# Kernel optimization log

Hardware: AMD Instinct MI355X
Metric: run time of the kernel (lower is better)

Reference implementation:

```python
import jax, jax.numpy as jnp
import numpy as np

NUM_HEADS = 8
NUM_POINTS = 4


def setup_inputs() -> dict:
    key = jax.random.key(0)
    ks = jax.random.split(key, 8)
    B, N, C, H, W = 8, 8192, 256, 128, 128
    HP2 = NUM_HEADS * NUM_POINTS * 2
    HP = NUM_HEADS * NUM_POINTS
    query = jax.random.normal(ks[0], (B, N, C), jnp.float32)
    reference_points = jax.random.uniform(ks[1], (B, N, 2), dtype=jnp.float32)
    value = jax.random.normal(ks[2], (B, C, H, W), jnp.float32)
    # learned params (offset gen is zero-init in the original; use small random
    W_off = jax.random.normal(ks[3], (C, HP2), jnp.float32) * 0.02
    b_off = jnp.zeros((HP2,), jnp.float32)
    W_attn = jax.random.normal(ks[4], (C, HP), jnp.float32) * (1.0 / np.sqrt(C))
    b_attn = jnp.zeros((HP,), jnp.float32)
    W_out = jax.random.normal(ks[5], (C, C), jnp.float32) * (1.0 / np.sqrt(C))
    b_out = jnp.zeros((C,), jnp.float32)
    return dict(query=query, reference_points=reference_points, value=value,
                W_off=W_off, b_off=b_off, W_attn=W_attn, b_attn=b_attn,
                W_out=W_out, b_out=b_out, H=H, W=W)


def reference(query, reference_points, value, W_off, b_off, W_attn, b_attn,
              W_out, b_out, H, W):
    B, N, C = query.shape
    Hh, P = NUM_HEADS, NUM_POINTS
    D = C // Hh

    offset = (query @ W_off + b_off).reshape(B, N, Hh, P, 2)
    attn = jax.nn.softmax((query @ W_attn + b_attn).reshape(B, N, Hh, P), axis=-1)

    # sampling locations in grid_sample convention: (x, y) in [-1, 1]
    ref = reference_points * 2.0 - 1.0
    loc = ref[:, :, None, None, :] + offset  # (B, N, Hh, P, 2)

    # value -> (B, Hh, H*W, D)
    val = value.reshape(B, Hh, D, H, W).transpose(0, 1, 3, 4, 2).reshape(B, Hh, H * W, D)

    # align_corners=False pixel coordinates
    x = (loc[..., 0] + 1.0) * (W * 0.5) - 0.5  # (B, N, Hh, P)
    y = (loc[..., 1] + 1.0) * (H * 0.5) - 0.5
    x0f = jnp.floor(x); y0f = jnp.floor(y)
    wx1 = x - x0f; wy1 = y - y0f
    x0 = x0f.astype(jnp.int32); y0 = y0f.astype(jnp.int32)
    x1 = x0 + 1; y1 = y0 + 1

    def gather(ix, iy, w):
        # bilinear corner gather with zero padding (mask out-of-bounds)
        valid = (ix >= 0) & (ix < W) & (iy >= 0) & (iy < H)
        idx = jnp.clip(iy, 0, H - 1) * W + jnp.clip(ix, 0, W - 1)  # (B,N,Hh,P)
        idx_t = idx.transpose(0, 2, 1, 3).reshape(B, Hh, N * P)
        g = jnp.take_along_axis(val, idx_t[..., None], axis=2)  # (B,Hh,N*P,D)
        g = g.reshape(B, Hh, N, P, D).transpose(0, 2, 1, 3, 4)  # (B,N,Hh,P,D)
        return g * (w * valid)[..., None]

    sampled = (gather(x0, y0, (1 - wx1) * (1 - wy1))
               + gather(x1, y0, wx1 * (1 - wy1))
               + gather(x0, y1, (1 - wx1) * wy1)
               + gather(x1, y1, wx1 * wy1))  # (B,N,Hh,P,D)

    out = jnp.einsum('bnhk,bnhkd->bnhd', attn, sampled).reshape(B, N, C)
    return out @ W_out + b_out
```

## Files before the change

### kernel.cpp

```cpp
#include <hip/hip_runtime.h>
#include <hip/hip_bf16.h>
#include <cstddef>

#define B_  8
#define N_  8192
#define C_  256
#define H_  128
#define W_  128
#define HH  8
#define PP  4
#define DD  32
#define HW  (H_ * W_)

typedef short bf16x8 __attribute__((ext_vector_type(8)));
typedef float f32x4  __attribute__((ext_vector_type(4)));

__global__ __launch_bounds__(256) void kT(const float* __restrict__ value,
                                          __hip_bfloat16* __restrict__ val) {
    __shared__ float tile[32][65];
    const int bh   = blockIdx.y;
    const int pix0 = blockIdx.x * 64;
    const int t    = threadIdx.x;

    const float* src = value + (size_t)bh * 32 * HW + pix0;
#pragma unroll
    for (int i = 0; i < 8; ++i) {
        int d = i * 4 + (t >> 6);
        int p = t & 63;
        tile[d][p] = src[(size_t)d * HW + p];
    }
    __syncthreads();
    __hip_bfloat162* dst =
        (__hip_bfloat162*)(val + ((size_t)bh * HW + pix0) * 32);
#pragma unroll
    for (int j = 0; j < 4; ++j) {
        int p  = j * 16 + (t >> 4);
        int dd = (t & 15) * 2;
        __hip_bfloat162 pk;
        pk.x = __float2bfloat16(tile[dd][p]);
        pk.y = __float2bfloat16(tile[dd + 1][p]);
        dst[p * 16 + (t & 15)] = pk;
    }
}

#define A1_BM 128
#define A1_BK 32

__global__ __launch_bounds__(256) void kA1(const float* __restrict__ query,
                                           const float* __restrict__ refp,
                                           const float* __restrict__ W_off,
                                           const float* __restrict__ b_off,
                                           const float* __restrict__ W_attn,
                                           const float* __restrict__ b_attn,
                                           float4* __restrict__ locattn) {
    __shared__ float At[A1_BK][A1_BM + 4];
    __shared__ float Bo[A1_BK][64];
    __shared__ float Ba[A1_BK][32];

    const int t    = threadIdx.x;
    const int row0 = blockIdx.x * A1_BM;
    const int rg   = t >> 3;
    const int h    = t & 7;

    float accO[4][8];
    float accA[4][4];
#pragma unroll
    for (int r = 0; r < 4; ++r) {
#pragma unroll
        for (int j = 0; j < 8; ++j) accO[r][j] = 0.f;
#pragma unroll
        for (int j = 0; j < 4; ++j) accA[r][j] = 0.f;
    }

    for (int k0 = 0; k0 < C_; k0 += A1_BK) {
        {
            int kq = (t & 7) * 4;
            int ra = t >> 3;
#pragma unroll
            for (int rr = 0; rr < 4; ++rr) {
                int r = ra + rr * 32;
                float4 q = *(const float4*)&query[(size_t)(row0 + r) * C_ + k0 + kq];
                At[kq + 0][r] = q.x;
                At[kq + 1][r] = q.y;
                At[kq + 2][r] = q.z;
                At[kq + 3][r] = q.w;
            }
        }
        {
            int c4 = (t & 15) * 4;
            int kb = t >> 4;
#pragma unroll
            for (int i = 0; i < 2; ++i) {
                int k = kb + i * 16;
                *(float4*)&Bo[k][c4] = *(const float4*)&W_off[(size_t)(k0 + k) * 64 + c4];
            }
        }
        {
            int c4 = (t & 7) * 4;
            int kb = t >> 3;
            *(float4*)&Ba[kb][c4] = *(const float4*)&W_attn[(size_t)(k0 + kb) * 32 + c4];
        }
        __syncthreads();

#pragma unroll
        for (int k = 0; k < A1_BK; ++k) {
            float4 a   = *(const float4*)&At[k][rg * 4];
            float4 bo0 = *(const float4*)&Bo[k][h * 8];
            float4 bo1 = *(const float4*)&Bo[k][h * 8 + 4];
            float4 ba  = *(const float4*)&Ba[k][h * 4];
            float av[4] = {a.x, a.y, a.z, a.w};
            float bO[8] = {bo0.x, bo0.y, bo0.z, bo0.w, bo1.x, bo1.y, bo1.z, bo1.w};
            float bA[4] = {ba.x, ba.y, ba.z, ba.w};
#pragma unroll
            for (int r = 0; r < 4; ++r) {
#pragma unroll
                for (int j = 0; j < 8; ++j) accO[r][j] += av[r] * bO[j];
#pragma unroll
                for (int j = 0; j < 4; ++j) accA[r][j] += av[r] * bA[j];
            }
        }
        __syncthreads();
    }

    float boff[8];
#pragma unroll
    for (int j = 0; j < 8; ++j) boff[j] = b_off[h * 8 + j];
    float batn[4];
#pragma unroll
    for (int j = 0; j < 4; ++j) batn[j] = b_attn[h * 4 + j];

#pragma unroll
    for (int r = 0; r < 4; ++r) {
        int row  = row0 + rg * 4 + r;
        int bb   = row >> 13;
        int nn   = row & 8191;
        float rx = refp[(size_t)row * 2 + 0];
        float ry = refp[(size_t)row * 2 + 1];
        float lg[4];
#pragma unroll
        for (int p = 0; p < 4; ++p) lg[p] = accA[r][p] + batn[p];
        float m = fmaxf(fmaxf(lg[0], lg[1]), fmaxf(lg[2], lg[3]));
        float e[4];
        float s = 0.f;
#pragma unroll
        for (int p = 0; p < 4; ++p) { e[p] = __expf(lg[p] - m); s += e[p]; }
        float inv = 1.f / s;
#pragma unroll
        for (int p = 0; p < 4; ++p) {
            float ox = accO[r][p * 2 + 0] + boff[p * 2 + 0];
            float oy = accO[r][p * 2 + 1] + boff[p * 2 + 1];
            float x  = (rx * 2.f + ox) * (W_ * 0.5f) - 0.5f;
            float y  = (ry * 2.f + oy) * (H_ * 0.5f) - 0.5f;
            locattn[(((size_t)bb * HH + h) * N_ + nn) * PP + p] =
                make_float4(x, y, e[p] * inv, 0.f);
        }
    }
}

__global__ __launch_bounds__(256) void kA2(const float4* __restrict__ locattn,
                                           const __hip_bfloat16* __restrict__ val,
                                           __hip_bfloat16* __restrict__ mid) {
    __shared__ float2 ow[64][4][4];

    const int t  = threadIdx.x;
    const int bh = blockIdx.y;
    const int b  = bh >> 3;
    const int h  = bh & 7;
    const int n0 = blockIdx.x * 64;

    {
        const int r = t >> 2;
        const int p = t & 3;
        float4 L = locattn[((size_t)bh * N_ + n0 + r) * PP + p];
        float x = L.x, y = L.y, a = L.z;
        float xf = floorf(x), yf = floorf(y);
        int x0 = (int)xf, y0 = (int)yf;
        int x1 = x0 + 1, y1 = y0 + 1;
        float wx1 = x - xf, wy1 = y - yf;
        float wx0 = 1.f - wx1, wy0 = 1.f - wy1;
        int cx0 = min(max(x0, 0), W_ - 1);
        int cx1 = min(max(x1, 0), W_ - 1);
        int cy0 = min(max(y0, 0), H_ - 1);
        int cy1 = min(max(y1, 0), H_ - 1);
        bool bx0 = (x0 >= 0) & (x0 < W_);
        bool bx1 = (x1 >= 0) & (x1 < W_);
        bool by0 = (y0 >= 0) & (y0 < H_);
        bool by1 = (y1 >= 0) & (y1 < H_);
        float w00 = a * wx0 * wy0 * ((bx0 & by0) ? 1.f : 0.f);
        float w10 = a * wx1 * wy0 * ((bx1 & by0) ? 1.f : 0.f);
        float w01 = a * wx0 * wy1 * ((bx0 & by1) ? 1.f : 0.f);
        float w11 = a * wx1 * wy1 * ((bx1 & by1) ? 1.f : 0.f);
        ow[r][p][0] = make_float2(__int_as_float(cy0 * W_ + cx0), w00);
        ow[r][p][1] = make_float2(__int_as_float(cy0 * W_ + cx1), w10);
        ow[r][p][2] = make_float2(__int_as_float(cy1 * W_ + cx0), w01);
        ow[r][p][3] = make_float2(__int_as_float(cy1 * W_ + cx1), w11);
    }
    __syncthreads();

    const int d  = t & 31;
    const int rg = t >> 5;
    const __hip_bfloat16* vb = val + (size_t)bh * HW * DD + d;
    __hip_bfloat16* mo = mid + ((size_t)b * N_ + n0) * C_ + h * DD + d;

#pragma unroll
    for (int j = 0; j < 8; ++j) {
        int r = rg * 8 + j;
        const float4* owp = (const float4*)&ow[r][0][0];
        float acc = 0.f;
#pragma unroll
        for (int p = 0; p < 4; ++p) {
            float4 u0 = owp[p * 2 + 0];
            float4 u1 = owp[p * 2 + 1];
            int o00 = __float_as_int(u0.x) * DD;
            int o10 = __float_as_int(u0.z) * DD;
            int o01 = __float_as_int(u1.x) * DD;
            int o11 = __float_as_int(u1.z) * DD;
            acc += u0.y * __bfloat162float(vb[o00]);
            acc += u0.w * __bfloat162float(vb[o10]);
            acc += u1.y * __bfloat162float(vb[o01]);
            acc += u1.w * __bfloat162float(vb[o11]);
        }
        mo[r * C_] = __float2bfloat16(acc);
    }
}

__global__ __launch_bounds__(256) void kW(const float* __restrict__ Wsrc,
                                          __hip_bfloat16* __restrict__ Wt) {
    __shared__ float tile[64][65];
    const int n0 = blockIdx.x * 64;
    const int k0 = blockIdx.y * 64;
    const int t  = threadIdx.x;
#pragma unroll
    for (int i = 0; i < 16; ++i) {
        int kk = i * 4 + (t >> 6);
        int nn = t & 63;
        tile[kk][nn] = Wsrc[(size_t)(k0 + kk) * 256 + n0 + nn];
    }
    __syncthreads();
#pragma unroll
    for (int i = 0; i < 16; ++i) {
        int nn = i * 4 + (t >> 6);
        int kk = t & 63;
        Wt[(size_t)(n0 + nn) * 256 + k0 + kk] = __float2bfloat16(tile[kk][nn]);
    }
}

__global__ __launch_bounds__(256) void kC(const short* __restrict__ mid,
                                          const short* __restrict__ Wt,
                                          const float* __restrict__ bias,
                                          float* __restrict__ out) {
    __shared__ __align__(16) short As[128 * 64];
    __shared__ __align__(16) short Bs[128 * 64];

    const int t    = threadIdx.x;
    const int lane = t & 63;
    const int w    = t >> 6;
    const int wm   = (w & 1) * 64;
    const int wn   = (w >> 1) * 64;
    const int row0 = blockIdx.x * 128;
    const int col0 = blockIdx.y * 128;

    f32x4 acc[4][4];
#pragma unroll
    for (int mt = 0; mt < 4; ++mt)
#pragma unroll
        for (int nt = 0; nt < 4; ++nt)
            acc[mt][nt] = (f32x4){0.f, 0.f, 0.f, 0.f};

    const int sr = t >> 3;
    const int kb = t & 7;

    for (int k0 = 0; k0 < 4; ++k0) {
#pragma unroll
        for (int i = 0; i < 4; ++i) {
            int row  = sr + i * 32;
            int kbs  = (kb ^ (row & 7)) * 8;
            *(uint4*)&As[row * 64 + kbs] =
                *(const uint4*)&mid[(size_t)(row0 + row) * 256 + k0 * 64 + kb * 8];
            *(uint4*)&Bs[row * 64 + kbs] =
                *(const uint4*)&Wt[(size_t)(col0 + row) * 256 + k0 * 64 + kb * 8];
        }
        __syncthreads();

#pragma unroll
        for (int ks = 0; ks < 2; ++ks) {
            const int kq = ks * 4 + (lane >> 4);
            bf16x8 af[4], bf[4];
#pragma unroll
            for (int mt = 0; mt < 4; ++mt) {
                int m = wm + mt * 16 + (lane & 15);
                af[mt] = *(const bf16x8*)&As[m * 64 + (kq ^ (m & 7)) * 8];
            }
#pragma unroll
            for (int nt = 0; nt < 4; ++nt) {
                int n = wn + nt * 16 + (lane & 15);
                bf[nt] = *(const bf16x8*)&Bs[n * 64 + (kq ^ (n & 7)) * 8];
            }
#pragma unroll
            for (int mt = 0; mt < 4; ++mt)
#pragma unroll
                for (int nt = 0; nt < 4; ++nt)
                    acc[mt][nt] = __builtin_amdgcn_mfma_f32_16x16x32_bf16(
                        af[mt], bf[nt], acc[mt][nt], 0, 0, 0);
        }
        __syncthreads();
    }

    const int cq = lane >> 4;
#pragma unroll
    for (int nt = 0; nt < 4; ++nt) {
        int col  = col0 + wn + nt * 16 + (lane & 15);
        float bv = bias[col];
#pragma unroll
        for (int mt = 0; mt < 4; ++mt) {
#pragma unroll
            for (int rI = 0; rI < 4; ++rI) {
                int rowg = row0 + wm + mt * 16 + cq * 4 + rI;
                out[(size_t)rowg * 256 + col] = acc[mt][nt][rI] + bv;
            }
        }
    }
}

extern "C" void kernel_launch(void* const* d_in, const int* in_sizes, int n_in,
                              void* d_out, int out_size, void* d_ws, size_t ws_size,
                              hipStream_t stream) {
    const float* query  = (const float*)d_in[0];
    const float* refp   = (const float*)d_in[1];
    const float* value  = (const float*)d_in[2];
    const float* W_off  = (const float*)d_in[3];
    const float* b_off  = (const float*)d_in[4];
    const float* W_attn = (const float*)d_in[5];
    const float* b_attn = (const float*)d_in[6];
    const float* W_out  = (const float*)d_in[7];
    const float* b_out  = (const float*)d_in[8];
    float* out = (float*)d_out;

    char*           ws      = (char*)d_ws;
    __hip_bfloat16* val     = (__hip_bfloat16*)(ws);
    float4*         locattn = (float4*)(ws + 67108864);
    __hip_bfloat16* mid     = (__hip_bfloat16*)(ws + 100663296);
    __hip_bfloat16* Wt      = (__hip_bfloat16*)(ws + 134217728);

    kT <<<dim3(HW / 64, B_ * HH), 256, 0, stream>>>(value, val);
    kW <<<dim3(4, 4), 256, 0, stream>>>(W_out, Wt);
    kA1<<<dim3((B_ * N_) / A1_BM), 256, 0, stream>>>(query, refp, W_off, b_off,
                                                     W_attn, b_attn, locattn);
    kA2<<<dim3(N_ / 64, B_ * HH), 256, 0, stream>>>(locattn, val, mid);
    kC <<<dim3((B_ * N_) / 128, C_ / 128), 256, 0, stream>>>(
        (const short*)mid, (const short*)Wt, b_out, out);
}
```

Baseline: 395.8 us.

## Move offset/attention projection GEMM to bf16x3 MFMA with split-precision weights

Replaces the scalar FP32 SIMT GEMM that computes sampling offsets and attention logits with an MFMA-based kernel. Query and weights are each split into bf16 hi and lo parts, and three MFMA products are accumulated to approximate FP32 accuracy. A new small kernel pre-splits and transposes the combined weights. Results are staged through swizzled LDS before the softmax and location epilogue. This trades extra conversion work and three MFMA passes for the much higher matrix-core throughput, which slightly changes precision.

```diff
diff --git a/kernel.cpp b/kernel.cpp
--- a/kernel.cpp
+++ b/kernel.cpp
@@ -15,6 +15,15 @@
 typedef short bf16x8 __attribute__((ext_vector_type(8)));
 typedef float f32x4  __attribute__((ext_vector_type(4)));
 
+static __device__ __forceinline__ short f2bf_s(float f) {
+    __hip_bfloat16 b = __float2bfloat16(f);
+    return *reinterpret_cast<short*>(&b);
+}
+static __device__ __forceinline__ float bf_s2f(short s) {
+    __hip_bfloat16 b = *reinterpret_cast<__hip_bfloat16*>(&s);
+    return __bfloat162float(b);
+}
+
 __global__ __launch_bounds__(256) void kT(const float* __restrict__ value,
                                           __hip_bfloat16* __restrict__ val) {
     __shared__ float tile[32][65];
@@ -43,85 +52,134 @@
     }
 }
 
-#define A1_BM 128
-#define A1_BK 32
-
-__global__ __launch_bounds__(256) void kA1(const float* __restrict__ query,
-                                           const float* __restrict__ refp,
-                                           const float* __restrict__ W_off,
-                                           const float* __restrict__ b_off,
-                                           const float* __restrict__ W_attn,
-                                           const float* __restrict__ b_attn,
-                                           float4* __restrict__ locattn) {
-    __shared__ float At[A1_BK][A1_BM + 4];
-    __shared__ float Bo[A1_BK][64];
-    __shared__ float Ba[A1_BK][32];
+__global__ __launch_bounds__(256) void kP(const float* __restrict__ W_off,
+                                          const float* __restrict__ W_attn,
+                                          short* __restrict__ Wc_hi,
+                                          short* __restrict__ Wc_lo) {
+    const int c = blockIdx.x;
+    const int k = threadIdx.x;
+    float v = (c < 64) ? W_off[(size_t)k * 64 + c]
+                       : W_attn[(size_t)k * 32 + (c - 64)];
+    short h = f2bf_s(v);
+    short l = f2bf_s(v - bf_s2f(h));
+    Wc_hi[(size_t)c * 256 + k] = h;
+    Wc_lo[(size_t)c * 256 + k] = l;
+}
+
+__global__ __launch_bounds__(256) void kA1M(const float* __restrict__ query,
+                                            const float* __restrict__ refp,
+                                            const short* __restrict__ Wc_hi,
+                                            const short* __restrict__ Wc_lo,
+                                            const float* __restrict__ b_off,
+                                            const float* __restrict__ b_attn,
+                                            float4* __restrict__ locattn) {
+    __shared__ __align__(16) char smem[57344];
+    short* As_hi = (short*)smem;
+    short* As_lo = (short*)(smem + 16384);
+    short* Bs_hi = (short*)(smem + 32768);
+    short* Bs_lo = (short*)(smem + 45056);
+    float* Ct    = (float*)smem;
 
     const int t    = threadIdx.x;
-    const int row0 = blockIdx.x * A1_BM;
-    const int rg   = t >> 3;
-    const int h    = t & 7;
-
-    float accO[4][8];
-    float accA[4][4];
-#pragma unroll
-    for (int r = 0; r < 4; ++r) {
-#pragma unroll
-        for (int j = 0; j < 8; ++j) accO[r][j] = 0.f;
-#pragma unroll
-        for (int j = 0; j < 4; ++j) accA[r][j] = 0.f;
-    }
-
-    for (int k0 = 0; k0 < C_; k0 += A1_BK) {
-        {
-            int kq = (t & 7) * 4;
-            int ra = t >> 3;
-#pragma unroll
-            for (int rr = 0; rr < 4; ++rr) {
-                int r = ra + rr * 32;
-                float4 q = *(const float4*)&query[(size_t)(row0 + r) * C_ + k0 + kq];
-                At[kq + 0][r] = q.x;
-                At[kq + 1][r] = q.y;
-                At[kq + 2][r] = q.z;
-                At[kq + 3][r] = q.w;
-            }
-        }
-        {
-            int c4 = (t & 15) * 4;
-            int kb = t >> 4;
-#pragma unroll
-            for (int i = 0; i < 2; ++i) {
-                int k = kb + i * 16;
-                *(float4*)&Bo[k][c4] = *(const float4*)&W_off[(size_t)(k0 + k) * 64 + c4];
-            }
-        }
-        {
-            int c4 = (t & 7) * 4;
-            int kb = t >> 3;
-            *(float4*)&Ba[kb][c4] = *(const float4*)&W_attn[(size_t)(k0 + kb) * 32 + c4];
+    const int lane = t & 63;
+    const int w    = t >> 6;
+    const int wm   = (w & 1) * 64;
+    const int wn   = (w >> 1) * 48;
+    const int quad = lane >> 4;
+    const int l16  = lane & 15;
+    const int row0 = blockIdx.x * 128;
+
+    f32x4 acc[4][3];
+#pragma unroll
+    for (int mt = 0; mt < 4; ++mt)
+#pragma unroll
+        for (int nt = 0; nt < 3; ++nt)
+            acc[mt][nt] = (f32x4){0.f, 0.f, 0.f, 0.f};
+
+    for (int k0c = 0; k0c < 4; ++k0c) {
+#pragma unroll
+        for (int i = 0; i < 8; ++i) {
+            int f   = t + i * 256;
+            int row = f >> 4;
+            int kq4 = f & 15;
+            float4 q = *(const float4*)&query[(size_t)(row0 + row) * 256 +
+                                              k0c * 64 + kq4 * 4];
+            short4 hv, lv;
+            hv.x = f2bf_s(q.x); lv.x = f2bf_s(q.x - bf_s2f(hv.x));
+            hv.y = f2bf_s(q.y); lv.y = f2bf_s(q.y - bf_s2f(hv.y));
+            hv.z = f2bf_s(q.z); lv.z = f2bf_s(q.z - bf_s2f(hv.z));
+            hv.w = f2bf_s(q.w); lv.w = f2bf_s(q.w - bf_s2f(hv.w));
+            int base = row * 64 + (((kq4 >> 1) ^ (row & 7)) * 8) + (kq4 & 1) * 4;
+            *(short4*)&As_hi[base] = hv;
+            *(short4*)&As_lo[base] = lv;
+        }
+#pragma unroll
+        for (int i = 0; i < 3; ++i) {
+            int idx = t + i * 256;
+            int n   = idx >> 3;
+            int kb  = idx & 7;
+            int dst = n * 64 + ((kb ^ (n & 7)) * 8);
+            *(uint4*)&Bs_hi[dst] =
+                *(const uint4*)&Wc_hi[(size_t)n * 256 + k0c * 64 + kb * 8];
+            *(uint4*)&Bs_lo[dst] =
+                *(const uint4*)&Wc_lo[(size_t)n * 256 + k0c * 64 + kb * 8];
         }
         __syncthreads();
 
 #pragma unroll
-        for (int k = 0; k < A1_BK; ++k) {
-            float4 a   = *(const float4*)&At[k][rg * 4];
-            float4 bo0 = *(const float4*)&Bo[k][h * 8];
-            float4 bo1 = *(const float4*)&Bo[k][h * 8 + 4];
-            float4 ba  = *(const float4*)&Ba[k][h * 4];
-            float av[4] = {a.x, a.y, a.z, a.w};
-            float bO[8] = {bo0.x, bo0.y, bo0.z, bo0.w, bo1.x, bo1.y, bo1.z, bo1.w};
-            float bA[4] = {ba.x, ba.y, ba.z, ba.w};
-#pragma unroll
-            for (int r = 0; r < 4; ++r) {
-#pragma unroll
-                for (int j = 0; j < 8; ++j) accO[r][j] += av[r] * bO[j];
-#pragma unroll
-                for (int j = 0; j < 4; ++j) accA[r][j] += av[r] * bA[j];
-            }
+        for (int ks = 0; ks < 2; ++ks) {
+            const int kq = ks * 4 + quad;
+            bf16x8 ah[4], al[4], bh[3], bl[3];
+#pragma unroll
+            for (int mt = 0; mt < 4; ++mt) {
+                int m = wm + mt * 16 + l16;
+                ah[mt] = *(const bf16x8*)&As_hi[m * 64 + (kq ^ (m & 7)) * 8];
+                al[mt] = *(const bf16x8*)&As_lo[m * 64 + (kq ^ (m & 7)) * 8];
+            }
+#pragma unroll
+            for (int nt = 0; nt < 3; ++nt) {
+                int n = wn + nt * 16 + l16;
+                bh[nt] = *(const bf16x8*)&Bs_hi[n * 64 + (kq ^ (n & 7)) * 8];
+                bl[nt] = *(const bf16x8*)&Bs_lo[n * 64 + (kq ^ (n & 7)) * 8];
+            }
+#pragma unroll
+            for (int mt = 0; mt < 4; ++mt)
+#pragma unroll
+                for (int nt = 0; nt < 3; ++nt)
+                    acc[mt][nt] = __builtin_amdgcn_mfma_f32_16x16x32_bf16(
+                        ah[mt], bh[nt], acc[mt][nt], 0, 0, 0);
+#pragma unroll
+            for (int mt = 0; mt < 4; ++mt)
+#pragma unroll
+                for (int nt = 0; nt < 3; ++nt)
+                    acc[mt][nt] = __builtin_amdgcn_mfma_f32_16x16x32_bf16(
+                        ah[mt], bl[nt], acc[mt][nt], 0, 0, 0);
+#pragma unroll
+            for (int mt = 0; mt < 4; ++mt)
+#pragma unroll
+                for (int nt = 0; nt < 3; ++nt)
+                    acc[mt][nt] = __builtin_amdgcn_mfma_f32_16x16x32_bf16(
+                        al[mt], bh[nt], acc[mt][nt], 0, 0, 0);
         }
         __syncthreads();
     }
 
+#pragma unroll
+    for (int mt = 0; mt < 4; ++mt) {
+#pragma unroll
+        for (int nt = 0; nt < 3; ++nt) {
+            int col = wn + nt * 16 + l16;
+#pragma unroll
+            for (int rI = 0; rI < 4; ++rI) {
+                int row = wm + mt * 16 + quad * 4 + rI;
+                Ct[row * 100 + col] = acc[mt][nt][rI];
+            }
+        }
+    }
+    __syncthreads();
+
+    const int rg = t >> 3;
+    const int h  = t & 7;
     float boff[8];
 #pragma unroll
     for (int j = 0; j < 8; ++j) boff[j] = b_off[h * 8 + j];
@@ -131,26 +189,31 @@
 
 #pragma unroll
     for (int r = 0; r < 4; ++r) {
-        int row  = row0 + rg * 4 + r;
-        int bb   = row >> 13;
-        int nn   = row & 8191;
-        float rx = refp[(size_t)row * 2 + 0];
-        float ry = refp[(size_t)row * 2 + 1];
-        float lg[4];
-#pragma unroll
-        for (int p = 0; p < 4; ++p) lg[p] = accA[r][p] + batn[p];
+        int row  = rg * 4 + r;
+        int rowg = row0 + row;
+        int bb   = rowg >> 13;
+        int nn   = rowg & 8191;
+        float rx = refp[(size_t)rowg * 2 + 0];
+        float ry = refp[(size_t)rowg * 2 + 1];
+        float4 lg4 = *(const float4*)&Ct[row * 100 + 64 + h * 4];
+        float lg[4] = {lg4.x + batn[0], lg4.y + batn[1],
+                       lg4.z + batn[2], lg4.w + batn[3]};
         float m = fmaxf(fmaxf(lg[0], lg[1]), fmaxf(lg[2], lg[3]));
         float e[4];
         float s = 0.f;
 #pragma unroll
         for (int p = 0; p < 4; ++p) { e[p] = __expf(lg[p] - m); s += e[p]; }
         float inv = 1.f / s;
+        float4 o0 = *(const float4*)&Ct[row * 100 + h * 8];
+        float4 o1 = *(const float4*)&Ct[row * 100 + h * 8 + 4];
+        float ox[4] = {o0.x + boff[0], o0.z + boff[2],
+                       o1.x + boff[4], o1.z + boff[6]};
+        float oy[4] = {o0.y + boff[1], o0.w + boff[3],
+                       o1.y + boff[5], o1.w + boff[7]};
 #pragma unroll
         for (int p = 0; p < 4; ++p) {
-            float ox = accO[r][p * 2 + 0] + boff[p * 2 + 0];
-            float oy = accO[r][p * 2 + 1] + boff[p * 2 + 1];
-            float x  = (rx * 2.f + ox) * (W_ * 0.5f) - 0.5f;
-            float y  = (ry * 2.f + oy) * (H_ * 0.5f) - 0.5f;
+            float x = (rx * 2.f + ox[p]) * (W_ * 0.5f) - 0.5f;
+            float y = (ry * 2.f + oy[p]) * (H_ * 0.5f) - 0.5f;
             locattn[(((size_t)bb * HH + h) * N_ + nn) * PP + p] =
                 make_float4(x, y, e[p] * inv, 0.f);
         }
@@ -341,12 +404,15 @@
     float4*         locattn = (float4*)(ws + 67108864);
     __hip_bfloat16* mid     = (__hip_bfloat16*)(ws + 100663296);
     __hip_bfloat16* Wt      = (__hip_bfloat16*)(ws + 134217728);
-
-    kT <<<dim3(HW / 64, B_ * HH), 256, 0, stream>>>(value, val);
-    kW <<<dim3(4, 4), 256, 0, stream>>>(W_out, Wt);
-    kA1<<<dim3((B_ * N_) / A1_BM), 256, 0, stream>>>(query, refp, W_off, b_off,
-                                                     W_attn, b_attn, locattn);
-    kA2<<<dim3(N_ / 64, B_ * HH), 256, 0, stream>>>(locattn, val, mid);
-    kC <<<dim3((B_ * N_) / 128, C_ / 128), 256, 0, stream>>>(
+    short*          Wc_hi   = (short*)(ws + 134348800);
+    short*          Wc_lo   = (short*)(ws + 134397952);
+
+    kT  <<<dim3(HW / 64, B_ * HH), 256, 0, stream>>>(value, val);
+    kP  <<<dim3(96), 256, 0, stream>>>(W_off, W_attn, Wc_hi, Wc_lo);
+    kW  <<<dim3(4, 4), 256, 0, stream>>>(W_out, Wt);
+    kA1M<<<dim3((B_ * N_) / 128), 256, 0, stream>>>(query, refp, Wc_hi, Wc_lo,
+                                                    b_off, b_attn, locattn);
+    kA2 <<<dim3(N_ / 64, B_ * HH), 256, 0, stream>>>(locattn, val, mid);
+    kC  <<<dim3((B_ * N_) / 128, C_ / 128), 256, 0, stream>>>(
         (const short*)mid, (const short*)Wt, b_out, out);
 }
```

New measurement: 381.3 us. 3.7% less time.
